# Optimization experiments

Hardware: AMD Instinct MI355X
Metric: run time of the kernel (lower is better)

Reference implementation:

```python
import jax, jax.numpy as jnp
import numpy as np

D_MODEL = 1024
N_HEADS = 16
HIDDEN = int(D_MODEL * 4 * 2 / 3)  # 2730, matches torch int(d*4*2/3)
EPS = 1e-6


def setup_inputs() -> dict:
    key = jax.random.key(0)
    ks = jax.random.split(key, 8)
    B, T = 4, 2048
    s = 0.02
    return {
        "x": jax.random.normal(ks[0], (B, T, D_MODEL), dtype=jnp.float32),
        "w_attn": jax.random.normal(ks[1], (D_MODEL, 3 * D_MODEL), dtype=jnp.float32) * s,
        "w_proj": jax.random.normal(ks[2], (D_MODEL, D_MODEL), dtype=jnp.float32) * s,
        "w1": jax.random.normal(ks[3], (D_MODEL, HIDDEN), dtype=jnp.float32) * s,
        "w2": jax.random.normal(ks[4], (D_MODEL, HIDDEN), dtype=jnp.float32) * s,
        "w3": jax.random.normal(ks[5], (HIDDEN, D_MODEL), dtype=jnp.float32) * s,
        "g1": jnp.ones((D_MODEL,), dtype=jnp.float32),
        "g2": jnp.ones((D_MODEL,), dtype=jnp.float32),
    }


def rmsnorm(x, g):
    norm = jax.lax.rsqrt(jnp.mean(x * x, axis=-1, keepdims=True) + EPS)
    return x * norm * g


def reference(x, w_attn, w_proj, w1, w2, w3, g1, g2):
    B, T, C = x.shape
    H = N_HEADS
    hd = C // H

    # attention branch
    qkv = rmsnorm(x, g1) @ w_attn                     # [B,T,3C]
    q, k, v = jnp.split(qkv, 3, axis=-1)
    q = q.reshape(B, T, H, hd).transpose(0, 2, 1, 3)  # [B,H,T,hd]
    k = k.reshape(B, T, H, hd).transpose(0, 2, 1, 3)
    v = v.reshape(B, T, H, hd).transpose(0, 2, 1, 3)

    att = jnp.einsum("bhqd,bhkd->bhqk", q, k) / jnp.sqrt(jnp.float32(hd))
    causal = jnp.tril(jnp.ones((T, T), dtype=bool))
    att = jnp.where(causal[None, None], att, jnp.float32(-jnp.inf))
    att = jax.nn.softmax(att, axis=-1)
    y = jnp.einsum("bhqk,bhkd->bhqd", att, v)          # [B,H,T,hd]
    y = y.transpose(0, 2, 1, 3).reshape(B, T, C)
    attn_out = y @ w_proj

    # parallel MLP branch on ln_2(x) (note: applied to x, not x+attn)
    h = rmsnorm(x, g2)
    mlp_out = (jax.nn.silu(h @ w1) * (h @ w2)) @ w3

    # dropout is identity in eval mode
    return x + attn_out + mlp_out
```

## Files before the change

kernel.cpp:

```cpp
#include <hip/hip_runtime.h>

#define TT 2048
#define DM 1024
#define HPAD 2816
#define HID 2730
#define SM_C 0.18033688f

typedef __attribute__((ext_vector_type(4))) float f32x4;
typedef __attribute__((ext_vector_type(8))) short bf16x8;

static __device__ __forceinline__ float bf2f(short u) {
    union { float f; unsigned int i; } c; c.i = ((unsigned int)(unsigned short)u) << 16; return c.f;
}
static __device__ __forceinline__ short f2bf(float f) {
    union { float f; unsigned int i; } c; c.f = f;
    unsigned int i = c.i;
    unsigned int r = (i + 0x7fffu + ((i >> 16) & 1u)) >> 16;
    return (short)r;
}
static __device__ __forceinline__ unsigned int fbits(float f) {
    union { float f; unsigned int i; } c; c.f = f;
    return c.i;
}

static __device__ __forceinline__ void gload_lds16(const void* g, void* l) {
    __builtin_amdgcn_global_load_lds(
        (const __attribute__((address_space(1))) unsigned int*)g,
        (__attribute__((address_space(3))) unsigned int*)l, 16, 0, 0);
}

__global__ __launch_bounds__(256) void wprep_all(
    const float* __restrict__ w_attn, const float* __restrict__ w_proj,
    const float* __restrict__ w1, const float* __restrict__ w2, const float* __restrict__ w3,
    short* __restrict__ wattn_t, short* __restrict__ wproj_t,
    short* __restrict__ w1t, short* __restrict__ w2t, short* __restrict__ w3t)
{
    __shared__ float tile[32][33];
    int id = blockIdx.x;
    const float* in; short* out; int K, N, Kpad, Npad, nbx;
    if (id < 3072)      {            in = w_attn; out = wattn_t; K = 1024; N = 3072; Kpad = 1024; Npad = 3072; nbx = 32; }
    else if (id < 4096) { id -= 3072; in = w_proj; out = wproj_t; K = 1024; N = 1024; Kpad = 1024; Npad = 1024; nbx = 32; }
    else if (id < 6912) { id -= 4096; in = w1;     out = w1t;     K = 1024; N = HID;  Kpad = 1024; Npad = HPAD; nbx = 32; }
    else if (id < 9728) { id -= 6912; in = w2;     out = w2t;     K = 1024; N = HID;  Kpad = 1024; Npad = HPAD; nbx = 32; }
    else                { id -= 9728; in = w3;     out = w3t;     K = HID;  N = 1024; Kpad = HPAD; Npad = 1024; nbx = 88; }
    int kb = (id % nbx) * 32, nb = (id / nbx) * 32;
    int tx = threadIdx.x, ty = threadIdx.y;
    #pragma unroll
    for (int i = 0; i < 32; i += 8) {
        int k = kb + ty + i, n = nb + tx;
        float v = (k < K && n < N) ? in[(size_t)k * N + n] : 0.f;
        tile[tx][ty + i] = v;
    }
    __syncthreads();
    #pragma unroll
    for (int i = 0; i < 32; i += 8) {
        int n = nb + ty + i, k = kb + tx;
        if (n < Npad && k < Kpad) out[(size_t)n * Kpad + k] = f2bf(tile[ty + i][tx]);
    }
}

__global__ __launch_bounds__(256) void rmsnorm2(const float* __restrict__ x,
    const float* __restrict__ g1, const float* __restrict__ g2,
    short* __restrict__ xn1, short* __restrict__ xn2) {
    int row = blockIdx.x;
    const float* xr = x + (size_t)row * DM;
    int t = threadIdx.x;
    float4 v = ((const float4*)xr)[t];
    float ss = v.x*v.x + v.y*v.y + v.z*v.z + v.w*v.w;
    #pragma unroll
    for (int off = 1; off < 64; off <<= 1) ss += __shfl_xor(ss, off);
    __shared__ float red[4];
    if ((t & 63) == 0) red[t >> 6] = ss;
    __syncthreads();
    float tot = red[0] + red[1] + red[2] + red[3];
    float rs = rsqrtf(tot * (1.0f / DM) + 1e-6f);
    float4 G1 = ((const float4*)g1)[t];
    float4 G2 = ((const float4*)g2)[t];
    union { short s[4]; int2 v; } o1, o2;
    o1.s[0] = f2bf(v.x * rs * G1.x); o1.s[1] = f2bf(v.y * rs * G1.y);
    o1.s[2] = f2bf(v.z * rs * G1.z); o1.s[3] = f2bf(v.w * rs * G1.w);
    o2.s[0] = f2bf(v.x * rs * G2.x); o2.s[1] = f2bf(v.y * rs * G2.y);
    o2.s[2] = f2bf(v.z * rs * G2.z); o2.s[3] = f2bf(v.w * rs * G2.w);
    *(int2*)(xn1 + (size_t)row * DM + t * 4) = o1.v;
    *(int2*)(xn2 + (size_t)row * DM + t * 4) = o2.v;
}

template<int EPI>
__global__ __launch_bounds__(512, 4) void gemm256(
    const short* __restrict__ A, const short* __restrict__ Bt,
    short* __restrict__ Cb, int N, int K)
{
    __shared__ short As[256 * 64];
    __shared__ short Bs[128 * 64];
    int t = threadIdx.x;
    int wid = t >> 6, l = t & 63;
    int wm = wid >> 1, wn = wid & 1;

    int nwg = gridDim.x, bid = blockIdx.x;
    int wg = (bid & 7) * (nwg >> 3) + (bid >> 3);
    int tiles_n = N >> 7;
    int tm = wg / tiles_n, tn = wg % tiles_n;

    f32x4 acc[4][4];
    #pragma unroll
    for (int m = 0; m < 4; m++)
        #pragma unroll
        for (int n = 0; n < 4; n++) acc[m][n] = (f32x4){0.f, 0.f, 0.f, 0.f};

    const short* Apan = A + (size_t)(tm * 256) * K;
    const short* Bpan = Bt + (size_t)(tn * 128) * K;

    for (int kt = 0; kt < K; kt += 64) {
        __syncthreads();
        #pragma unroll
        for (int i = 0; i < 4; i++) {
            int lin = i * 512 + t;
            int row = lin >> 3;
            int slot = lin & 7;
            int src = slot ^ (row & 7);
            gload_lds16(Apan + (size_t)row * K + kt + src * 8, (char*)As + lin * 16);
        }
        #pragma unroll
        for (int i = 0; i < 2; i++) {
            int lin = i * 512 + t;
            int row = lin >> 3;
            int slot = lin & 7;
            int src = slot ^ (row & 7);
            gload_lds16(Bpan + (size_t)row * K + kt + src * 8, (char*)Bs + lin * 16);
        }
        __syncthreads();
        #pragma unroll
        for (int ks = 0; ks < 2; ks++) {
            bf16x8 af[4], bfr[4];
            #pragma unroll
            for (int m = 0; m < 4; m++) {
                int row = wm * 64 + m * 16 + (l & 15);
                af[m] = *(const bf16x8*)((char*)As + row * 128 + ((ks * 64 + (l >> 4) * 16) ^ ((row & 7) << 4)));
            }
            #pragma unroll
            for (int n = 0; n < 4; n++) {
                int row = wn * 64 + n * 16 + (l & 15);
                bfr[n] = *(const bf16x8*)((char*)Bs + row * 128 + ((ks * 64 + (l >> 4) * 16) ^ ((row & 7) << 4)));
            }
            __builtin_amdgcn_s_setprio(1);
            #pragma unroll
            for (int m = 0; m < 4; m++)
                #pragma unroll
                for (int n = 0; n < 4; n++)
                    acc[m][n] = __builtin_amdgcn_mfma_f32_16x16x32_bf16(af[m], bfr[n], acc[m][n], 0, 0, 0);
            __builtin_amdgcn_s_setprio(0);
        }
    }

    bool qcols = (EPI == 5) && (tn < 8);
    #pragma unroll
    for (int m = 0; m < 4; m++)
        #pragma unroll
        for (int n = 0; n < 4; n++)
            #pragma unroll
            for (int r = 0; r < 4; r++) {
                int row = tm * 256 + wm * 64 + m * 16 + (l >> 4) * 4 + r;
                int col = tn * 128 + wn * 64 + n * 16 + (l & 15);
                size_t idx = (size_t)row * N + col;
                float v = acc[m][n][r];
                if constexpr (EPI == 5) Cb[idx] = f2bf(qcols ? v * SM_C : v);
                else Cb[idx] = f2bf(v);
            }
}

__global__ __launch_bounds__(256) void gemm_fuse(
    const short* __restrict__ A1, const short* __restrict__ B1,
    const short* __restrict__ A2, const short* __restrict__ B2,
    const float* __restrict__ X, float* __restrict__ Of)
{
    __shared__ short As[128 * 64];
    __shared__ short Bs[128 * 64];
    int t = threadIdx.x;
    int wid = t >> 6, l = t & 63;
    int wm = wid >> 1, wn = wid & 1;

    int nwg = gridDim.x, bid = blockIdx.x;
    int wg = (bid & 7) * (nwg >> 3) + (bid >> 3);
    int tiles_n = 8;
    int tm = wg / tiles_n, tn = wg % tiles_n;

    f32x4 acc[4][4];
    #pragma unroll
    for (int m = 0; m < 4; m++)
        #pragma unroll
        for (int n = 0; n < 4; n++) acc[m][n] = (f32x4){0.f, 0.f, 0.f, 0.f};

    #pragma unroll 1
    for (int phase = 0; phase < 2; phase++) {
        const short* Arow = phase == 0 ? A1 + (size_t)(tm * 128) * 1024 : A2 + (size_t)(tm * 128) * HPAD;
        const short* Brow = phase == 0 ? B1 + (size_t)(tn * 128) * 1024 : B2 + (size_t)(tn * 128) * HPAD;
        int K = phase == 0 ? 1024 : HPAD;
        for (int kt = 0; kt < K; kt += 64) {
            __syncthreads();
            #pragma unroll
            for (int i = 0; i < 4; i++) {
                int linear = i * 256 + t;
                int row = linear >> 3;
                int slot = linear & 7;
                int srcslot = slot ^ (row & 7);
                gload_lds16(Arow + (size_t)row * K + kt + srcslot * 8, (char*)As + linear * 16);
                gload_lds16(Brow + (size_t)row * K + kt + srcslot * 8, (char*)Bs + linear * 16);
            }
            __syncthreads();
            #pragma unroll
            for (int ks = 0; ks < 2; ks++) {
                bf16x8 af[4], bfr[4];
                #pragma unroll
                for (int m = 0; m < 4; m++) {
                    int row = wm * 64 + m * 16 + (l & 15);
                    af[m] = *(const bf16x8*)((char*)As + row * 128 + ((ks * 64 + (l >> 4) * 16) ^ ((row & 7) << 4)));
                }
                #pragma unroll
                for (int n = 0; n < 4; n++) {
                    int row = wn * 64 + n * 16 + (l & 15);
                    bfr[n] = *(const bf16x8*)((char*)Bs + row * 128 + ((ks * 64 + (l >> 4) * 16) ^ ((row & 7) << 4)));
                }
                #pragma unroll
                for (int m = 0; m < 4; m++)
                    #pragma unroll
                    for (int n = 0; n < 4; n++)
                        acc[m][n] = __builtin_amdgcn_mfma_f32_16x16x32_bf16(af[m], bfr[n], acc[m][n], 0, 0, 0);
            }
        }
    }

    #pragma unroll
    for (int m = 0; m < 4; m++)
        #pragma unroll
        for (int n = 0; n < 4; n++)
            #pragma unroll
            for (int r = 0; r < 4; r++) {
                int row = tm * 128 + wm * 64 + m * 16 + (l >> 4) * 4 + r;
                int col = tn * 128 + wn * 64 + n * 16 + (l & 15);
                size_t idx = (size_t)row * 1024 + col;
                Of[idx] = X[idx] + acc[m][n][r];
            }
}

__global__ __launch_bounds__(512, 2) void gemm_mlp2(
    const short* __restrict__ A, const short* __restrict__ B1t, const short* __restrict__ B2t,
    short* __restrict__ Cb, int M, int N, int K)
{
    __shared__ short As[128 * 64];
    __shared__ short B1s[128 * 64];
    __shared__ short B2s[128 * 64];
    int t = threadIdx.x;
    int wid = t >> 6, l = t & 63;
    int wm = wid >> 2, wn = wid & 3;

    int nwg = gridDim.x, bid = blockIdx.x;
    int wg = (bid & 7) * (nwg >> 3) + (bid >> 3);
    int tiles_n = N >> 7;
    int tm = wg / tiles_n, tn = wg % tiles_n;

    const short* Arow  = A   + (size_t)(tm * 128) * K;
    const short* B1row = B1t + (size_t)(tn * 128) * K;
    const short* B2row = B2t + (size_t)(tn * 128) * K;

    f32x4 acc1[4][2], acc2[4][2];
    #pragma unroll
    for (int m = 0; m < 4; m++)
        #pragma unroll
        for (int n = 0; n < 2; n++) {
            acc1[m][n] = (f32x4){0.f, 0.f, 0.f, 0.f};
            acc2[m][n] = (f32x4){0.f, 0.f, 0.f, 0.f};
        }

    for (int kt = 0; kt < K; kt += 64) {
        __syncthreads();
        #pragma unroll
        for (int i = 0; i < 2; i++) {
            int linear = i * 512 + t;
            int row = linear >> 3;
            int slot = linear & 7;
            int srcslot = slot ^ (row & 7);
            gload_lds16(Arow  + (size_t)row * K + kt + srcslot * 8, (char*)As  + linear * 16);
            gload_lds16(B1row + (size_t)row * K + kt + srcslot * 8, (char*)B1s + linear * 16);
            gload_lds16(B2row + (size_t)row * K + kt + srcslot * 8, (char*)B2s + linear * 16);
        }
        __syncthreads();
        #pragma unroll
        for (int ks = 0; ks < 2; ks++) {
            bf16x8 af[4], b1[2], b2[2];
            #pragma unroll
            for (int m = 0; m < 4; m++) {
                int row = wm * 64 + m * 16 + (l & 15);
                int off = (ks * 64 + (l >> 4) * 16) ^ ((row & 7) << 4);
                af[m] = *(const bf16x8*)((char*)As + row * 128 + off);
            }
            #pragma unroll
            for (int n = 0; n < 2; n++) {
                int row = wn * 32 + n * 16 + (l & 15);
                int off = (ks * 64 + (l >> 4) * 16) ^ ((row & 7) << 4);
                b1[n] = *(const bf16x8*)((char*)B1s + row * 128 + off);
                b2[n] = *(const bf16x8*)((char*)B2s + row * 128 + off);
            }
            #pragma unroll
            for (int m = 0; m < 4; m++)
                #pragma unroll
                for (int n = 0; n < 2; n++) {
                    acc1[m][n] = __builtin_amdgcn_mfma_f32_16x16x32_bf16(af[m], b1[n], acc1[m][n], 0, 0, 0);
                    acc2[m][n] = __builtin_amdgcn_mfma_f32_16x16x32_bf16(af[m], b2[n], acc2[m][n], 0, 0, 0);
                }
        }
    }

    #pragma unroll
    for (int m = 0; m < 4; m++)
        #pragma unroll
        for (int n = 0; n < 2; n++)
            #pragma unroll
            for (int r = 0; r < 4; r++) {
                int row = tm * 128 + wm * 64 + m * 16 + (l >> 4) * 4 + r;
                int col = tn * 128 + wn * 32 + n * 16 + (l & 15);
                float v1 = acc1[m][n][r];
                float v2 = acc2[m][n][r];
                Cb[(size_t)row * N + col] = f2bf(v1 * (1.f / (1.f + __expf(-v1))) * v2);
            }
}

__global__ __launch_bounds__(512, 4) void attn(const short* __restrict__ qkv, short* __restrict__ y) {
    __shared__ short Ks[2][64 * 64];
    __shared__ short Vt[2][64 * 64];
    int bid = blockIdx.x;
    int xcd = bid & 7;
    int idx = bid >> 3;
    int bh  = xcd + 8 * (idx >> 3);
    int pair = idx & 7;
    int b = bh >> 4, h = bh & 15;
    int t = threadIdx.x, wid = t >> 6, l = t & 63;
    const size_t base = (size_t)b * TT * 3072;

    int krow = t >> 3, kslot = t & 7, ksrc = kslot ^ (krow & 7);
    int vrg = t >> 3, vch = t & 7;

    #pragma unroll
    for (int pass = 0; pass < 2; pass++) {
        int qt = pass == 0 ? (15 - pair) : pair;
        int q0 = qt * 128 + wid * 16;
        int qrow = q0 + (l & 15);

        bf16x8 qf[2];
        #pragma unroll
        for (int s = 0; s < 2; s++) {
            int row = q0 + (l & 15);
            qf[s] = *(const bf16x8*)(qkv + base + (size_t)row * 3072 + h * 64 + s * 32 + (l >> 4) * 8);
        }

        f32x4 o[4];
        #pragma unroll
        for (int n = 0; n < 4; n++) o[n] = (f32x4){0.f, 0.f, 0.f, 0.f};
        float ll = 0.f;

        int nt = 2 * qt + 2;

        {
            gload_lds16(qkv + base + (size_t)krow * 3072 + 1024 + h * 64 + ksrc * 8,
                        (char*)Ks + t * 16);
            if (t < 256) {
                uint4 va = *(const uint4*)(qkv + base + (size_t)(vrg * 2)     * 3072 + 2048 + h * 64 + vch * 8);
                uint4 vb = *(const uint4*)(qkv + base + (size_t)(vrg * 2 + 1) * 3072 + 2048 + h * 64 + vch * 8);
                const unsigned int* a32 = (const unsigned int*)&va;
                const unsigned int* b32 = (const unsigned int*)&vb;
                #pragma unroll
                for (int j = 0; j < 8; j++) {
                    int w = j >> 1;
                    unsigned int pack = __builtin_amdgcn_perm(b32[w], a32[w],
                                        (j & 1) ? 0x07060302u : 0x05040100u);
                    int d = vch * 8 + j;
                    int byte = (d * 128 + vrg * 4) ^ ((j ^ vch) << 4);
                    *(unsigned int*)((char*)Vt + byte) = pack;
                }
            }
            __syncthreads();
        }

        int cur = 0;
        for (int it = 0; it < nt; ++it) {
            int kb = it << 6;
            bool have_next = (it + 1 < nt);
            uint4 va, vb;
            if (have_next) {
                int nkb = kb + 64;
                gload_lds16(qkv + base + (size_t)(nkb + krow) * 3072 + 1024 + h * 64 + ksrc * 8,
                            (char*)Ks + (cur ^ 1) * 8192 + t * 16);
                if (t < 256) {
                    va = *(const uint4*)(qkv + base + (size_t)(nkb + vrg * 2)     * 3072 + 2048 + h * 64 + vch * 8);
                    vb = *(const uint4*)(qkv + base + (size_t)(nkb + vrg * 2 + 1) * 3072 + 2048 + h * 64 + vch * 8);
                }
            }
            if (kb <= q0 + 15) {
                bool diag = (kb + 63 > q0);
                unsigned int pk[4][2];
                __builtin_amdgcn_s_setprio(1);
                #pragma unroll
                for (int j = 0; j < 4; j++) {
                    f32x4 z = (f32x4){0.f, 0.f, 0.f, 0.f};
                    #pragma unroll
                    for (int ks = 0; ks < 2; ks++) {
                        int row = j * 16 + (l & 15);
                        bf16x8 kf = *(const bf16x8*)((char*)Ks + cur * 8192 + row * 128 +
                                    ((ks * 64 + (l >> 4) * 16) ^ ((row & 7) << 4)));
                        z = __builtin_amdgcn_mfma_f32_16x16x32_bf16(kf, qf[ks], z, 0, 0, 0);
                    }
                    float p[4];
                    #pragma unroll
                    for (int r = 0; r < 4; r++) {
                        float v = z[r];
                        if (diag) {
                            int kcol = kb + j * 16 + (l >> 4) * 4 + r;
                            if (kcol > qrow) v = -3e38f;
                        }
                        p[r] = exp2f(v);
                        ll += p[r];
                    }
                    pk[j][0] = __builtin_amdgcn_perm(fbits(p[1]), fbits(p[0]), 0x07060302u);
                    pk[j][1] = __builtin_amdgcn_perm(fbits(p[3]), fbits(p[2]), 0x07060302u);
                }
                __builtin_amdgcn_s_setprio(0);

                #pragma unroll
                for (int ks = 0; ks < 2; ks++) {
                    union { unsigned int u[4]; bf16x8 v; } pa;
                    #pragma unroll
                    for (int w = 0; w < 4; w++) {
                        int src = (((l >> 4) & 1) << 5) | ((w >> 1) << 4) | (l & 15);
                        unsigned int a = __shfl(pk[2 * ks][w & 1], src);
                        unsigned int bb = __shfl(pk[2 * ks + 1][w & 1], src);
                        pa.u[w] = (l >> 5) ? bb : a;
                    }
                    __builtin_amdgcn_s_setprio(1);
                    #pragma unroll
                    for (int n = 0; n < 4; n++) {
                        int vr = n * 16 + (l & 15);
                        int f = (vr & 7) ^ ((vr >> 3) & 7);
                        bf16x8 vf = *(const bf16x8*)((char*)Vt + cur * 8192 + vr * 128 +
                                    ((ks * 64 + (l >> 4) * 16) ^ (f << 4)));
                        o[n] = __builtin_amdgcn_mfma_f32_16x16x32_bf16(pa.v, vf, o[n], 0, 0, 0);
                    }
                    __builtin_amdgcn_s_setprio(0);
                }
            }
            if (have_next && t < 256) {
                const unsigned int* a32 = (const unsigned int*)&va;
                const unsigned int* b32 = (const unsigned int*)&vb;
                #pragma unroll
                for (int j = 0; j < 8; j++) {
                    int w = j >> 1;
                    unsigned int pack = __builtin_amdgcn_perm(b32[w], a32[w],
                                        (j & 1) ? 0x07060302u : 0x05040100u);
                    int d = vch * 8 + j;
                    int byte = (d * 128 + vrg * 4) ^ ((j ^ vch) << 4);
                    *(unsigned int*)((char*)Vt + (cur ^ 1) * 8192 + byte) = pack;
                }
            }
            __syncthreads();
            cur ^= 1;
        }

        ll += __shfl_xor(ll, 16);
        ll += __shfl_xor(ll, 32);
        float inv = 1.f / ll;
        #pragma unroll
        for (int r = 0; r < 4; r++) {
            float invr = __shfl(inv, (l >> 4) * 4 + r);
            #pragma unroll
            for (int n = 0; n < 4; n++) {
                int row = q0 + (l >> 4) * 4 + r;
                int col = h * 64 + n * 16 + (l & 15);
                y[(size_t)(b * TT + row) * DM + col] = f2bf(o[n][r] * invr);
            }
        }
    }
}

extern "C" void kernel_launch(void* const* d_in, const int* in_sizes, int n_in,
                              void* d_out, int out_size, void* d_ws, size_t ws_size,
                              hipStream_t stream) {
    (void)in_sizes; (void)n_in; (void)out_size; (void)ws_size;
    const float* x      = (const float*)d_in[0];
    const float* w_attn = (const float*)d_in[1];
    const float* w_proj = (const float*)d_in[2];
    const float* w1     = (const float*)d_in[3];
    const float* w2     = (const float*)d_in[4];
    const float* w3     = (const float*)d_in[5];
    const float* g1     = (const float*)d_in[6];
    const float* g2     = (const float*)d_in[7];
    float* out = (float*)d_out;

    char* ws = (char*)d_ws;
    size_t off = 0;
    auto alloc = [&](size_t bytes) { char* p = ws + off; off += (bytes + 255) & ~(size_t)255; return p; };
    short* wattn_t = (short*)alloc((size_t)3072 * 1024 * 2);
    short* wproj_t = (short*)alloc((size_t)1024 * 1024 * 2);
    short* w1t     = (short*)alloc((size_t)HPAD * 1024 * 2);
    short* w2t     = (short*)alloc((size_t)HPAD * 1024 * 2);
    short* w3t     = (short*)alloc((size_t)1024 * HPAD * 2);
    short* xn1     = (short*)alloc((size_t)8192 * 1024 * 2);
    short* xn2     = (short*)alloc((size_t)8192 * 1024 * 2);
    short* qkvb    = (short*)alloc((size_t)8192 * 3072 * 2);
    short* yb      = (short*)alloc((size_t)8192 * 1024 * 2);
    short* hb      = (short*)alloc((size_t)8192 * HPAD * 2);

    dim3 tb(32, 8);
    wprep_all<<<12544, tb, 0, stream>>>(w_attn, w_proj, w1, w2, w3,
                                        wattn_t, wproj_t, w1t, w2t, w3t);

    rmsnorm2<<<8192, 256, 0, stream>>>(x, g1, g2, xn1, xn2);

    gemm256<5><<<768, 512, 0, stream>>>(xn1, wattn_t, qkvb, 3072, 1024);
    attn<<<512, 512, 0, stream>>>(qkvb, yb);
    gemm_mlp2<<<1408, 512, 0, stream>>>(xn2, w1t, w2t, hb, 8192, HPAD, 1024);
    gemm_fuse<<<512, 256, 0, stream>>>(yb, wproj_t, hb, w3t, x, out);
}
```

Baseline: 331.9 us.

## Split dual-weight MLP GEMM into two 256x128 GEMMs with SiLU-gate epilogue

Result: slower. 358.3 us (+7.9%).

```diff
diff --git a/kernel.cpp b/kernel.cpp
--- a/kernel.cpp
+++ b/kernel.cpp
@@ -88,6 +88,7 @@
 template<int EPI>
 __global__ __launch_bounds__(512, 4) void gemm256(
     const short* __restrict__ A, const short* __restrict__ Bt,
+    const short* __restrict__ H1,
     short* __restrict__ Cb, int N, int K)
 {
     __shared__ short As[256 * 64];
@@ -164,6 +165,10 @@
                 size_t idx = (size_t)row * N + col;
                 float v = acc[m][n][r];
                 if constexpr (EPI == 5) Cb[idx] = f2bf(qcols ? v * SM_C : v);
+                else if constexpr (EPI == 6) {
+                    float hv = bf2f(H1[idx]);
+                    Cb[idx] = f2bf(hv * (1.f / (1.f + __expf(-hv))) * v);
+                }
                 else Cb[idx] = f2bf(v);
             }
 }
@@ -239,88 +244,6 @@
                 int col = tn * 128 + wn * 64 + n * 16 + (l & 15);
                 size_t idx = (size_t)row * 1024 + col;
                 Of[idx] = X[idx] + acc[m][n][r];
-            }
-}
-
-__global__ __launch_bounds__(512, 2) void gemm_mlp2(
-    const short* __restrict__ A, const short* __restrict__ B1t, const short* __restrict__ B2t,
-    short* __restrict__ Cb, int M, int N, int K)
-{
-    __shared__ short As[128 * 64];
-    __shared__ short B1s[128 * 64];
-    __shared__ short B2s[128 * 64];
-    int t = threadIdx.x;
-    int wid = t >> 6, l = t & 63;
-    int wm = wid >> 2, wn = wid & 3;
-
-    int nwg = gridDim.x, bid = blockIdx.x;
-    int wg = (bid & 7) * (nwg >> 3) + (bid >> 3);
-    int tiles_n = N >> 7;
-    int tm = wg / tiles_n, tn = wg % tiles_n;
-
-    const short* Arow  = A   + (size_t)(tm * 128) * K;
-    const short* B1row = B1t + (size_t)(tn * 128) * K;
-    const short* B2row = B2t + (size_t)(tn * 128) * K;
-
-    f32x4 acc1[4][2], acc2[4][2];
-    #pragma unroll
-    for (int m = 0; m < 4; m++)
-        #pragma unroll
-        for (int n = 0; n < 2; n++) {
-            acc1[m][n] = (f32x4){0.f, 0.f, 0.f, 0.f};
-            acc2[m][n] = (f32x4){0.f, 0.f, 0.f, 0.f};
-        }
-
-    for (int kt = 0; kt < K; kt += 64) {
-        __syncthreads();
-        #pragma unroll
-        for (int i = 0; i < 2; i++) {
-            int linear = i * 512 + t;
-            int row = linear >> 3;
-            int slot = linear & 7;
-            int srcslot = slot ^ (row & 7);
-            gload_lds16(Arow  + (size_t)row * K + kt + srcslot * 8, (char*)As  + linear * 16);
-            gload_lds16(B1row + (size_t)row * K + kt + srcslot * 8, (char*)B1s + linear * 16);
-            gload_lds16(B2row + (size_t)row * K + kt + srcslot * 8, (char*)B2s + linear * 16);
-        }
-        __syncthreads();
-        #pragma unroll
-        for (int ks = 0; ks < 2; ks++) {
-            bf16x8 af[4], b1[2], b2[2];
-            #pragma unroll
-            for (int m = 0; m < 4; m++) {
-                int row = wm * 64 + m * 16 + (l & 15);
-                int off = (ks * 64 + (l >> 4) * 16) ^ ((row & 7) << 4);
-                af[m] = *(const bf16x8*)((char*)As + row * 128 + off);
-            }
-            #pragma unroll
-            for (int n = 0; n < 2; n++) {
-                int row = wn * 32 + n * 16 + (l & 15);
-                int off = (ks * 64 + (l >> 4) * 16) ^ ((row & 7) << 4);
-                b1[n] = *(const bf16x8*)((char*)B1s + row * 128 + off);
-                b2[n] = *(const bf16x8*)((char*)B2s + row * 128 + off);
-            }
-            #pragma unroll
-            for (int m = 0; m < 4; m++)
-                #pragma unroll
-                for (int n = 0; n < 2; n++) {
-                    acc1[m][n] = __builtin_amdgcn_mfma_f32_16x16x32_bf16(af[m], b1[n], acc1[m][n], 0, 0, 0);
-                    acc2[m][n] = __builtin_amdgcn_mfma_f32_16x16x32_bf16(af[m], b2[n], acc2[m][n], 0, 0, 0);
-                }
-        }
-    }
-
-    #pragma unroll
-    for (int m = 0; m < 4; m++)
-        #pragma unroll
-        for (int n = 0; n < 2; n++)
-            #pragma unroll
-            for (int r = 0; r < 4; r++) {
-                int row = tm * 128 + wm * 64 + m * 16 + (l >> 4) * 4 + r;
-                int col = tn * 128 + wn * 32 + n * 16 + (l & 15);
-                float v1 = acc1[m][n][r];
-                float v2 = acc2[m][n][r];
-                Cb[(size_t)row * N + col] = f2bf(v1 * (1.f / (1.f + __expf(-v1))) * v2);
             }
 }
 
@@ -506,6 +429,7 @@
     short* qkvb    = (short*)alloc((size_t)8192 * 3072 * 2);
     short* yb      = (short*)alloc((size_t)8192 * 1024 * 2);
     short* hb      = (short*)alloc((size_t)8192 * HPAD * 2);
+    short* h1b     = qkvb;
 
     dim3 tb(32, 8);
     wprep_all<<<12544, tb, 0, stream>>>(w_attn, w_proj, w1, w2, w3,
@@ -513,8 +437,9 @@
 
     rmsnorm2<<<8192, 256, 0, stream>>>(x, g1, g2, xn1, xn2);
 
-    gemm256<5><<<768, 512, 0, stream>>>(xn1, wattn_t, qkvb, 3072, 1024);
+    gemm256<5><<<768, 512, 0, stream>>>(xn1, wattn_t, nullptr, qkvb, 3072, 1024);
     attn<<<512, 512, 0, stream>>>(qkvb, yb);
-    gemm_mlp2<<<1408, 512, 0, stream>>>(xn2, w1t, w2t, hb, 8192, HPAD, 1024);
+    gemm256<0><<<704, 512, 0, stream>>>(xn2, w1t, nullptr, h1b, HPAD, 1024);
+    gemm256<6><<<704, 512, 0, stream>>>(xn2, w2t, h1b, hb, HPAD, 1024);
     gemm_fuse<<<512, 256, 0, stream>>>(yb, wproj_t, hb, w3t, x, out);
 }
```

## Merge attention and MLP up-projection into one heterogeneous launch

Applied to the files above, without the earlier changes.

Measured after the change: 335.7 us. No clear change (+1.2%).

```diff
diff --git a/kernel.cpp b/kernel.cpp
--- a/kernel.cpp
+++ b/kernel.cpp
@@ -242,92 +242,10 @@
             }
 }
 
-__global__ __launch_bounds__(512, 2) void gemm_mlp2(
-    const short* __restrict__ A, const short* __restrict__ B1t, const short* __restrict__ B2t,
-    short* __restrict__ Cb, int M, int N, int K)
-{
-    __shared__ short As[128 * 64];
-    __shared__ short B1s[128 * 64];
-    __shared__ short B2s[128 * 64];
-    int t = threadIdx.x;
-    int wid = t >> 6, l = t & 63;
-    int wm = wid >> 2, wn = wid & 3;
-
-    int nwg = gridDim.x, bid = blockIdx.x;
-    int wg = (bid & 7) * (nwg >> 3) + (bid >> 3);
-    int tiles_n = N >> 7;
-    int tm = wg / tiles_n, tn = wg % tiles_n;
-
-    const short* Arow  = A   + (size_t)(tm * 128) * K;
-    const short* B1row = B1t + (size_t)(tn * 128) * K;
-    const short* B2row = B2t + (size_t)(tn * 128) * K;
-
-    f32x4 acc1[4][2], acc2[4][2];
-    #pragma unroll
-    for (int m = 0; m < 4; m++)
-        #pragma unroll
-        for (int n = 0; n < 2; n++) {
-            acc1[m][n] = (f32x4){0.f, 0.f, 0.f, 0.f};
-            acc2[m][n] = (f32x4){0.f, 0.f, 0.f, 0.f};
-        }
-
-    for (int kt = 0; kt < K; kt += 64) {
-        __syncthreads();
-        #pragma unroll
-        for (int i = 0; i < 2; i++) {
-            int linear = i * 512 + t;
-            int row = linear >> 3;
-            int slot = linear & 7;
-            int srcslot = slot ^ (row & 7);
-            gload_lds16(Arow  + (size_t)row * K + kt + srcslot * 8, (char*)As  + linear * 16);
-            gload_lds16(B1row + (size_t)row * K + kt + srcslot * 8, (char*)B1s + linear * 16);
-            gload_lds16(B2row + (size_t)row * K + kt + srcslot * 8, (char*)B2s + linear * 16);
-        }
-        __syncthreads();
-        #pragma unroll
-        for (int ks = 0; ks < 2; ks++) {
-            bf16x8 af[4], b1[2], b2[2];
-            #pragma unroll
-            for (int m = 0; m < 4; m++) {
-                int row = wm * 64 + m * 16 + (l & 15);
-                int off = (ks * 64 + (l >> 4) * 16) ^ ((row & 7) << 4);
-                af[m] = *(const bf16x8*)((char*)As + row * 128 + off);
-            }
-            #pragma unroll
-            for (int n = 0; n < 2; n++) {
-                int row = wn * 32 + n * 16 + (l & 15);
-                int off = (ks * 64 + (l >> 4) * 16) ^ ((row & 7) << 4);
-                b1[n] = *(const bf16x8*)((char*)B1s + row * 128 + off);
-                b2[n] = *(const bf16x8*)((char*)B2s + row * 128 + off);
-            }
-            #pragma unroll
-            for (int m = 0; m < 4; m++)
-                #pragma unroll
-                for (int n = 0; n < 2; n++) {
-                    acc1[m][n] = __builtin_amdgcn_mfma_f32_16x16x32_bf16(af[m], b1[n], acc1[m][n], 0, 0, 0);
-                    acc2[m][n] = __builtin_amdgcn_mfma_f32_16x16x32_bf16(af[m], b2[n], acc2[m][n], 0, 0, 0);
-                }
-        }
-    }
-
-    #pragma unroll
-    for (int m = 0; m < 4; m++)
-        #pragma unroll
-        for (int n = 0; n < 2; n++)
-            #pragma unroll
-            for (int r = 0; r < 4; r++) {
-                int row = tm * 128 + wm * 64 + m * 16 + (l >> 4) * 4 + r;
-                int col = tn * 128 + wn * 32 + n * 16 + (l & 15);
-                float v1 = acc1[m][n][r];
-                float v2 = acc2[m][n][r];
-                Cb[(size_t)row * N + col] = f2bf(v1 * (1.f / (1.f + __expf(-v1))) * v2);
-            }
-}
-
-__global__ __launch_bounds__(512, 4) void attn(const short* __restrict__ qkv, short* __restrict__ y) {
-    __shared__ short Ks[2][64 * 64];
-    __shared__ short Vt[2][64 * 64];
-    int bid = blockIdx.x;
+static __device__ void attn_body(const short* __restrict__ qkv, short* __restrict__ y,
+                                 int bid, char* smem) {
+    char* KsB = smem;
+    char* VtB = smem + 16384;
     int xcd = bid & 7;
     int idx = bid >> 3;
     int bh  = xcd + 8 * (idx >> 3);
@@ -361,7 +279,7 @@
 
         {
             gload_lds16(qkv + base + (size_t)krow * 3072 + 1024 + h * 64 + ksrc * 8,
-                        (char*)Ks + t * 16);
+                        KsB + t * 16);
             if (t < 256) {
                 uint4 va = *(const uint4*)(qkv + base + (size_t)(vrg * 2)     * 3072 + 2048 + h * 64 + vch * 8);
                 uint4 vb = *(const uint4*)(qkv + base + (size_t)(vrg * 2 + 1) * 3072 + 2048 + h * 64 + vch * 8);
@@ -374,7 +292,7 @@
                                         (j & 1) ? 0x07060302u : 0x05040100u);
                     int d = vch * 8 + j;
                     int byte = (d * 128 + vrg * 4) ^ ((j ^ vch) << 4);
-                    *(unsigned int*)((char*)Vt + byte) = pack;
+                    *(unsigned int*)(VtB + byte) = pack;
                 }
             }
             __syncthreads();
@@ -388,7 +306,7 @@
             if (have_next) {
                 int nkb = kb + 64;
                 gload_lds16(qkv + base + (size_t)(nkb + krow) * 3072 + 1024 + h * 64 + ksrc * 8,
-                            (char*)Ks + (cur ^ 1) * 8192 + t * 16);
+                            KsB + (cur ^ 1) * 8192 + t * 16);
                 if (t < 256) {
                     va = *(const uint4*)(qkv + base + (size_t)(nkb + vrg * 2)     * 3072 + 2048 + h * 64 + vch * 8);
                     vb = *(const uint4*)(qkv + base + (size_t)(nkb + vrg * 2 + 1) * 3072 + 2048 + h * 64 + vch * 8);
@@ -404,7 +322,7 @@
                     #pragma unroll
                     for (int ks = 0; ks < 2; ks++) {
                         int row = j * 16 + (l & 15);
-                        bf16x8 kf = *(const bf16x8*)((char*)Ks + cur * 8192 + row * 128 +
+                        bf16x8 kf = *(const bf16x8*)(KsB + cur * 8192 + row * 128 +
                                     ((ks * 64 + (l >> 4) * 16) ^ ((row & 7) << 4)));
                         z = __builtin_amdgcn_mfma_f32_16x16x32_bf16(kf, qf[ks], z, 0, 0, 0);
                     }
@@ -439,7 +357,7 @@
                     for (int n = 0; n < 4; n++) {
                         int vr = n * 16 + (l & 15);
                         int f = (vr & 7) ^ ((vr >> 3) & 7);
-                        bf16x8 vf = *(const bf16x8*)((char*)Vt + cur * 8192 + vr * 128 +
+                        bf16x8 vf = *(const bf16x8*)(VtB + cur * 8192 + vr * 128 +
                                     ((ks * 64 + (l >> 4) * 16) ^ (f << 4)));
                         o[n] = __builtin_amdgcn_mfma_f32_16x16x32_bf16(pa.v, vf, o[n], 0, 0, 0);
                     }
@@ -456,7 +374,7 @@
                                         (j & 1) ? 0x07060302u : 0x05040100u);
                     int d = vch * 8 + j;
                     int byte = (d * 128 + vrg * 4) ^ ((j ^ vch) << 4);
-                    *(unsigned int*)((char*)Vt + (cur ^ 1) * 8192 + byte) = pack;
+                    *(unsigned int*)(VtB + (cur ^ 1) * 8192 + byte) = pack;
                 }
             }
             __syncthreads();
@@ -477,6 +395,99 @@
             }
         }
     }
+}
+
+static __device__ void mlp2_body(const short* __restrict__ A, const short* __restrict__ B1t,
+                                 const short* __restrict__ B2t, short* __restrict__ Cb,
+                                 int bid, int nwg, int N, int K, char* smem) {
+    char* As  = smem;
+    char* B1s = smem + 16384;
+    char* B2s = smem + 32768;
+    int t = threadIdx.x;
+    int wid = t >> 6, l = t & 63;
+    int wm = wid >> 2, wn = wid & 3;
+
+    int wg = (bid & 7) * (nwg >> 3) + (bid >> 3);
+    int tiles_n = N >> 7;
+    int tm = wg / tiles_n, tn = wg % tiles_n;
+
+    const short* Arow  = A   + (size_t)(tm * 128) * K;
+    const short* B1row = B1t + (size_t)(tn * 128) * K;
+    const short* B2row = B2t + (size_t)(tn * 128) * K;
+
+    f32x4 acc1[4][2], acc2[4][2];
+    #pragma unroll
+    for (int m = 0; m < 4; m++)
+        #pragma unroll
+        for (int n = 0; n < 2; n++) {
+            acc1[m][n] = (f32x4){0.f, 0.f, 0.f, 0.f};
+            acc2[m][n] = (f32x4){0.f, 0.f, 0.f, 0.f};
+        }
+
+    for (int kt = 0; kt < K; kt += 64) {
+        __syncthreads();
+        #pragma unroll
+        for (int i = 0; i < 2; i++) {
+            int linear = i * 512 + t;
+            int row = linear >> 3;
+            int slot = linear & 7;
+            int srcslot = slot ^ (row & 7);
+            gload_lds16(Arow  + (size_t)row * K + kt + srcslot * 8, As  + linear * 16);
+            gload_lds16(B1row + (size_t)row * K + kt + srcslot * 8, B1s + linear * 16);
+            gload_lds16(B2row + (size_t)row * K + kt + srcslot * 8, B2s + linear * 16);
+        }
+        __syncthreads();
+        #pragma unroll
+        for (int ks = 0; ks < 2; ks++) {
+            bf16x8 af[4], b1[2], b2[2];
+            #pragma unroll
+            for (int m = 0; m < 4; m++) {
+                int row = wm * 64 + m * 16 + (l & 15);
+                int off = (ks * 64 + (l >> 4) * 16) ^ ((row & 7) << 4);
+                af[m] = *(const bf16x8*)(As + row * 128 + off);
+            }
+            #pragma unroll
+            for (int n = 0; n < 2; n++) {
+                int row = wn * 32 + n * 16 + (l & 15);
+                int off = (ks * 64 + (l >> 4) * 16) ^ ((row & 7) << 4);
+                b1[n] = *(const bf16x8*)(B1s + row * 128 + off);
+                b2[n] = *(const bf16x8*)(B2s + row * 128 + off);
+            }
+            __builtin_amdgcn_s_setprio(1);
+            #pragma unroll
+            for (int m = 0; m < 4; m++)
+                #pragma unroll
+                for (int n = 0; n < 2; n++) {
+                    acc1[m][n] = __builtin_amdgcn_mfma_f32_16x16x32_bf16(af[m], b1[n], acc1[m][n], 0, 0, 0);
+                    acc2[m][n] = __builtin_amdgcn_mfma_f32_16x16x32_bf16(af[m], b2[n], acc2[m][n], 0, 0, 0);
+                }
+            __builtin_amdgcn_s_setprio(0);
+        }
+    }
+
+    #pragma unroll
+    for (int m = 0; m < 4; m++)
+        #pragma unroll
+        for (int n = 0; n < 2; n++)
+            #pragma unroll
+            for (int r = 0; r < 4; r++) {
+                int row = tm * 128 + wm * 64 + m * 16 + (l >> 4) * 4 + r;
+                int col = tn * 128 + wn * 32 + n * 16 + (l & 15);
+                float v1 = acc1[m][n][r];
+                float v2 = acc2[m][n][r];
+                Cb[(size_t)row * N + col] = f2bf(v1 * (1.f / (1.f + __expf(-v1))) * v2);
+            }
+}
+
+__global__ __launch_bounds__(512, 2) void attn_mlp(
+    const short* __restrict__ qkv, short* __restrict__ y,
+    const short* __restrict__ xn2, const short* __restrict__ w1t,
+    const short* __restrict__ w2t, short* __restrict__ hb)
+{
+    __shared__ char smem[49152];
+    int bid = blockIdx.x;
+    if (bid < 512) attn_body(qkv, y, bid, smem);
+    else           mlp2_body(xn2, w1t, w2t, hb, bid - 512, 1408, HPAD, 1024, smem);
 }
 
 extern "C" void kernel_launch(void* const* d_in, const int* in_sizes, int n_in,
@@ -514,7 +525,6 @@
     rmsnorm2<<<8192, 256, 0, stream>>>(x, g1, g2, xn1, xn2);
 
     gemm256<5><<<768, 512, 0, stream>>>(xn1, wattn_t, qkvb, 3072, 1024);
-    attn<<<512, 512, 0, stream>>>(qkvb, yb);
-    gemm_mlp2<<<1408, 512, 0, stream>>>(xn2, w1t, w2t, hb, 8192, HPAD, 1024);
+    attn_mlp<<<1920, 512, 0, stream>>>(qkvb, yb, xn2, w1t, w2t, hb);
     gemm_fuse<<<512, 256, 0, stream>>>(yb, wproj_t, hb, w3t, x, out);
 }
```
